# Performance work log

Hardware: AMD Instinct MI355X
Metric: run time of the kernel (lower is better)

## Reference

```python
import jax, jax.numpy as jnp
import numpy as np

T_STEPS = 500
NHEAD = 4
L_TRANS = 2

def _pe(L, D):
    pos = np.arange(L)[:, None].astype(np.float32)
    i = np.arange(D // 2)[None, :].astype(np.float32)
    ang = pos / np.power(10000.0, 2.0 * i / D)
    pe = np.zeros((L, D), np.float32)
    pe[:, 0::2] = np.sin(ang)
    pe[:, 1::2] = np.cos(ang)
    return jnp.asarray(pe)

def _ln(x, g, b):
    m = x.mean(-1, keepdims=True)
    v = ((x - m) ** 2).mean(-1, keepdims=True)
    return (x - m) / jnp.sqrt(v + 1e-5) * g + b

def _gcn(A, X, W1, b1, W2, b2, W3, b3):
    h = jax.nn.relu((A @ X) @ W1 + b1)
    h = jax.nn.relu((A @ h) @ W2 + b2)
    return (A @ h) @ W3 + b3

def _mha(h, Wq, bq, Wk, bk, Wv, bv, Wo, bo):
    B, L, D = h.shape
    dh = D // NHEAD
    q = (h @ Wq + bq).reshape(B, L, NHEAD, dh)
    k = (h @ Wk + bk).reshape(B, L, NHEAD, dh)
    v = (h @ Wv + bv).reshape(B, L, NHEAD, dh)
    s = jnp.einsum('blhd,bmhd->bhlm', q, k) / jnp.sqrt(jnp.float32(dh))
    a = jax.nn.softmax(s, axis=-1)
    o = jnp.einsum('bhlm,bmhd->blhd', a, v).reshape(B, L, D)
    return o @ Wo + bo


def setup_inputs() -> dict:
    key = jax.random.key(0)
    ks = jax.random.split(key, 24)
    N_FP, N_WORD, DIM, HID = 10000, 4096, 20, 512
    HD1, HD2, LOUT, TDIM, FF = 128, 64, 3, 20, 2048
    N_ATOMS, N_RES, N_EDGES = 256, 4096, 65536
    w = lambda k, shp, s=0.05: jax.random.normal(k, shp, jnp.float32) * s
    idx_aa = jax.random.randint(ks[0], (N_RES,), 0, 20)
    x = jax.nn.one_hot(idx_aa, 20, dtype=jnp.float32)  # node one-hots
    adj_s = (jax.random.uniform(ks[1], (N_ATOMS, N_ATOMS)) < 0.1).astype(jnp.float32)
    return dict(
        x=x,
        smileadjacency=adj_s,
        emb_fp=w(ks[2], (N_FP, DIM)),
        emb_word=w(ks[3], (N_WORD, HID), 0.02),
        gW1=w(ks[4], (DIM, HD1)), gb1=jnp.zeros((HD1,), jnp.float32),
        gW2=w(ks[5], (HD1, HD2)), gb2=jnp.zeros((HD2,), jnp.float32),
        gW3=w(ks[6], (HD2, DIM)), gb3=jnp.zeros((DIM,), jnp.float32),
        Wq=w(ks[7], (L_TRANS, HID, HID)), bq=jnp.zeros((L_TRANS, HID), jnp.float32),
        Wk=w(ks[8], (L_TRANS, HID, HID)), bk=jnp.zeros((L_TRANS, HID), jnp.float32),
        Wv=w(ks[9], (L_TRANS, HID, HID)), bv=jnp.zeros((L_TRANS, HID), jnp.float32),
        Wo=w(ks[10], (L_TRANS, HID, HID)), bo=jnp.zeros((L_TRANS, HID), jnp.float32),
        ln1g=jnp.ones((L_TRANS, HID), jnp.float32), ln1b=jnp.zeros((L_TRANS, HID), jnp.float32),
        Wff1=w(ks[11], (L_TRANS, HID, FF)), bff1=jnp.zeros((L_TRANS, FF), jnp.float32),
        Wff2=w(ks[12], (L_TRANS, FF, HID)), bff2=jnp.zeros((L_TRANS, HID), jnp.float32),
        ln2g=jnp.ones((L_TRANS, HID), jnp.float32), ln2b=jnp.zeros((L_TRANS, HID), jnp.float32),
        Wproj=w(ks[13], (HID, DIM)), bproj=jnp.zeros((DIM,), jnp.float32),
        Wout=w(ks[14], (LOUT, 4 * DIM, 4 * DIM)), bout=jnp.zeros((LOUT, 4 * DIM), jnp.float32),
        Wtime=w(ks[15], (1, TDIM)), btime=jnp.zeros((TDIM,), jnp.float32),
        fingerprints=jax.random.randint(ks[16], (N_ATOMS,), 0, N_FP),
        words=jax.random.randint(ks[17], (N_RES,), 0, N_WORD),
        batch=jnp.zeros((N_RES,), jnp.int32),
        edge_index=jax.random.randint(ks[18], (2, N_EDGES), 0, N_RES),
        t=250,
        layer_output=3,
        dropout=0,
    )


def reference(x, smileadjacency, emb_fp, emb_word, gW1, gb1, gW2, gb2, gW3, gb3,
              Wq, bq, Wk, bk, Wv, bv, Wo, bo, ln1g, ln1b, Wff1, bff1, Wff2, bff2,
              ln2g, ln2b, Wproj, bproj, Wout, bout, Wtime, btime,
              fingerprints, words, batch, edge_index, t, layer_output, dropout):
    # --- diffusion noise (cosine alpha_bar, blosum-style transition, uniform mixing) ---
    t_float = float(t) / T_STEPS
    s = 0.008
    ab = np.cos((t_float + s) / (1 + s) * np.pi / 2) ** 2 / (np.cos(s / (1 + s) * np.pi / 2) ** 2)
    ab = jnp.float32(ab)
    Qtb = ab * jnp.eye(20, dtype=jnp.float32) + (1.0 - ab) / 20.0  # [20,20]
    prob = jnp.einsum('nij,nj->ni', Qtb[None][batch], x[:, :20])    # [n,20]
    X_t = jax.random.categorical(jax.random.key(42), jnp.log(prob + 1e-9))
    X = jax.nn.one_hot(X_t, 20, dtype=jnp.float32)
    time_emb = jnp.array([[t_float]], jnp.float32) @ Wtime + btime  # [1,20]
    # --- substrate GCN ---
    fp_vec = emb_fp[fingerprints]                                   # [n_atoms, dim]
    sub = _gcn(smileadjacency, fp_vec, gW1, gb1, gW2, gb2, gW3, gb3).mean(0, keepdims=True)
    # --- sequence transformer ---
    h = emb_word[words][None] + _pe(words.shape[0], emb_word.shape[1])[None]  # [1,L,hid]
    for l in range(L_TRANS):
        a = _mha(h, Wq[l], bq[l], Wk[l], bk[l], Wv[l], bv[l], Wo[l], bo[l])
        h = _ln(h + a, ln1g[l], ln1b[l])
        ff = jax.nn.relu(h @ Wff1[l] + bff1[l]) @ Wff2[l] + bff2[l]
        h = _ln(h + ff, ln2g[l], ln2b[l])
    seq = (h[0] @ Wproj + bproj).mean(0, keepdims=True)             # [1,dim]
    # --- protein graph: vectorized adjacency scatter (replaces per-edge python loop) ---
    n = X.shape[0]
    adj = jnp.zeros((n, n), jnp.float32).at[edge_index[0], edge_index[1]].set(1.0)
    prot = _gcn(adj, X, gW1, gb1, gW2, gb2, gW3, gb3).mean(0, keepdims=True)
    # --- fusion head (dropout=0 / eval mode) ---
    cat = jnp.concatenate([sub, prot, seq, time_emb], axis=1)        # [1, 4*dim]
    for j in range(int(layer_output)):
        cat = jax.nn.relu(cat) @ Wout[j] + bout[j]
    cat = jax.nn.relu(cat)
    return (cat, seq)
```

## Files before the change

kernel.cpp:

```cpp
#include <hip/hip_runtime.h>
#include <math.h>

typedef unsigned short ushort_t;
typedef __attribute__((ext_vector_type(8))) short bf16x8;
typedef __attribute__((ext_vector_type(4))) float f32x4;

__device__ inline float bf2f(unsigned u) { return __uint_as_float((u & 0xffffu) << 16); }
__device__ inline ushort_t f2bf(float f) {
    unsigned u = __float_as_uint(f);
    return (ushort_t)((u + 0x7fffu + ((u >> 16) & 1u)) >> 16);
}
__device__ inline unsigned pack2(float a, float b) {
    return (unsigned)f2bf(a) | ((unsigned)f2bf(b) << 16);
}
__device__ inline void stv(float* p, float v) { *p = v; }
__device__ inline void stv(ushort_t* p, float v) { *p = f2bf(v); }
__device__ inline int guard_int(int raw, int lo, int hi) {
    if (raw >= lo && raw <= hi) return raw;
    float f = __int_as_float(raw);
    int v = (int)f;
    return (v >= lo && v <= hi) ? v : lo;
}

__device__ inline void tf2x32(unsigned k0, unsigned k1, unsigned x0, unsigned x1,
                              unsigned& o0, unsigned& o1) {
    unsigned ks2 = k0 ^ k1 ^ 0x1BD11BDAu;
    x0 += k0; x1 += k1;
#define TFR(r) { x0 += x1; x1 = (x1 << (r)) | (x1 >> (32 - (r))); x1 ^= x0; }
    TFR(13) TFR(15) TFR(26) TFR(6)  x0 += k1;  x1 += ks2 + 1u;
    TFR(17) TFR(29) TFR(16) TFR(24) x0 += ks2; x1 += k0 + 2u;
    TFR(13) TFR(15) TFR(26) TFR(6)  x0 += k0;  x1 += k1 + 3u;
    TFR(17) TFR(29) TFR(16) TFR(24) x0 += k1;  x1 += ks2 + 4u;
    TFR(13) TFR(15) TFR(26) TFR(6)  x0 += ks2; x1 += k0 + 5u;
#undef TFR
    o0 = x0; o1 = x1;
}

__global__ void k_sentinel(float* __restrict__ out, float val, int n) {
    int i = blockIdx.x * 128 + threadIdx.x;
    if (i < n) out[i] = val;
}

__global__ __launch_bounds__(256) void k_sample(const float* __restrict__ x,
                                                const int* __restrict__ t_ptr,
                                                float* __restrict__ X) {
    int i = blockIdx.x * 256 + threadIdx.x;
    if (i >= 4096) return;
    int tval = guard_int(t_ptr[0], 0, 500);
    double tf = (double)tval / 500.0;
    const double sc = 0.008;
    const double PI_HALF = 1.5707963267948966;
    double num = cos((tf + sc) / (1.0 + sc) * PI_HALF);
    double den = cos(sc / (1.0 + sc) * PI_HALF);
    float ab = (float)((num * num) / (den * den));
    float phi = (1.0f - ab) / 20.0f;
    float xv[20]; float sx = 0.f;
    for (int j = 0; j < 20; ++j) { xv[j] = x[i * 20 + j]; sx += xv[j]; }
    float best = -1e30f; int bj = 0;
    for (int j = 0; j < 20; ++j) {
        float prob = fmaxf(ab * xv[j] + phi * sx, 0.0f);
        float lp = logf(prob + 1e-9f);
        unsigned m = (unsigned)(i * 20 + j);
        unsigned o0, o1;
        tf2x32(0u, 42u, 0u, m, o0, o1);
        unsigned bits = o0 ^ o1;
        float u = __uint_as_float((bits >> 9) | 0x3f800000u) - 1.0f;
        if (u < 1.1754943508222875e-38f) u = 1.1754943508222875e-38f;
        float gmb = -logf(-logf(u));
        float z = lp + gmb;
        if (z > best) { best = z; bj = j; }
    }
    for (int j = 0; j < 20; ++j) X[i * 20 + j] = (j == bj) ? 1.0f : 0.0f;
}

__global__ __launch_bounds__(256) void k_gather_fp(const float* __restrict__ emb,
                                                   const int* __restrict__ idx,
                                                   float* __restrict__ out) {
    int i = blockIdx.x * 256 + threadIdx.x;
    if (i >= 256 * 20) return;
    int a = i / 20, d = i % 20;
    out[i] = emb[(size_t)idx[a] * 20 + d];
}

__global__ __launch_bounds__(256) void k_scatter_bits(const int* __restrict__ ei,
                                                      unsigned* __restrict__ bits) {
    int e = blockIdx.x * 256 + threadIdx.x;
    if (e >= 65536) return;
    int r = ei[e], c = ei[65536 + e];
    atomicOr(&bits[(size_t)r * 128 + (c >> 5)], 1u << (c & 31));
}

__global__ __launch_bounds__(256) void k_degree(const unsigned* __restrict__ BITS,
                                                float* __restrict__ deg) {
    int i = blockIdx.x * 256 + threadIdx.x;
    if (i >= 4096 * 128) return;
    unsigned bits = BITS[i];
    int base = (i & 127) * 32;
    while (bits) { int b = __ffs(bits) - 1; bits &= bits - 1; atomicAdd(&deg[base + b], 1.0f); }
}

__global__ __launch_bounds__(256) void k_embed(const float* __restrict__ embw,
                                               const int* __restrict__ words,
                                               float* __restrict__ H,
                                               ushort_t* __restrict__ Hb) {
    int idx = blockIdx.x * 256 + threadIdx.x;
    if (idx >= 4096 * 512) return;
    int pos = idx >> 9, d = idx & 511;
    float e = embw[(size_t)words[pos] * 512 + d];
    float expo = (float)(d >> 1) * (1.0f / 256.0f);
    float ang = (float)pos * exp2f(-expo * 13.287712379549449f);
    float pe = (d & 1) ? cosf(ang) : sinf(ang);
    float v = e + pe;
    H[idx] = v; Hb[idx] = f2bf(v);
}

__global__ __launch_bounds__(256) void k_colmean(const float* __restrict__ M, int R, int C,
                                                 float* __restrict__ out) {
    __shared__ float red[256];
    int c = blockIdx.x, t = threadIdx.x;
    float s = 0.f;
    for (int r = t; r < R; r += 256) s += M[(size_t)r * C + c];
    red[t] = s; __syncthreads();
    for (int o = 128; o; o >>= 1) { if (t < o) red[t] += red[t + o]; __syncthreads(); }
    if (t == 0) out[c] = red[0] / (float)R;
}

__global__ __launch_bounds__(256) void k_wcolsum(const float* __restrict__ M, int R, int C,
                                                 const float* __restrict__ w,
                                                 float* __restrict__ out) {
    __shared__ float red[256];
    int c = blockIdx.x, t = threadIdx.x;
    float s = 0.f;
    for (int r = t; r < R; r += 256) s += w[r] * M[(size_t)r * C + c];
    red[t] = s; __syncthreads();
    for (int o = 128; o; o >>= 1) { if (t < o) red[t] += red[t + o]; __syncthreads(); }
    if (t == 0) out[c] = red[0];
}

__global__ __launch_bounds__(256) void k_matvec20(int D, float scale,
                                                  const float* __restrict__ vec,
                                                  const float* __restrict__ W,
                                                  const float* __restrict__ bias,
                                                  float* __restrict__ out) {
    __shared__ float red[256];
    int c = blockIdx.x, t = threadIdx.x;
    float s = 0.f;
    for (int d = t; d < D; d += 256) s += vec[d] * W[(size_t)d * 20 + c];
    red[t] = s; __syncthreads();
    for (int o = 128; o; o >>= 1) { if (t < o) red[t] += red[t + o]; __syncthreads(); }
    if (t == 0) out[c] = red[0] * scale + bias[c];
}

__global__ void k_gather3(const float* __restrict__ a, const float* __restrict__ b,
                          const float* __restrict__ c, float* __restrict__ out) {
    int i = blockIdx.x * 256 + threadIdx.x;
    if (i >= 1536) return;
    out[i] = (i < 512) ? a[i] : (i < 1024) ? b[i - 512] : c[i - 1024];
}

__global__ __launch_bounds__(256) void k_castT(const float* __restrict__ in,
                                               ushort_t* __restrict__ out,
                                               int Kd, int Nd) {
    __shared__ float t[32][33];
    int bx = blockIdx.x * 32, by = blockIdx.y * 32;
    int tx = threadIdx.x & 31, ty = threadIdx.x >> 5;
#pragma unroll
    for (int i = 0; i < 4; ++i)
        t[ty + i * 8][tx] = in[(size_t)(by + ty + i * 8) * Nd + bx + tx];
    __syncthreads();
#pragma unroll
    for (int i = 0; i < 4; ++i)
        out[(size_t)(bx + ty + i * 8) * Kd + by + tx] = f2bf(t[tx][ty + i * 8]);
}

__global__ __launch_bounds__(256) void k_castT4(const float* __restrict__ in0,
                                                const float* __restrict__ in1,
                                                const float* __restrict__ in2,
                                                const float* __restrict__ in3,
                                                ushort_t* __restrict__ out) {
    __shared__ float t[32][33];
    int z = blockIdx.z;
    const float* in = (z == 0) ? in0 : (z == 1) ? in1 : (z == 2) ? in2 : in3;
    ushort_t* o = out + (size_t)z * 262144;
    int bx = blockIdx.x * 32, by = blockIdx.y * 32;
    int tx = threadIdx.x & 31, ty = threadIdx.x >> 5;
#pragma unroll
    for (int i = 0; i < 4; ++i)
        t[ty + i * 8][tx] = in[(size_t)(by + ty + i * 8) * 512 + bx + tx];
    __syncthreads();
#pragma unroll
    for (int i = 0; i < 4; ++i)
        o[(size_t)(bx + ty + i * 8) * 512 + by + tx] = f2bf(t[tx][ty + i * 8]);
}

template<int BN, bool RELU, bool VTR, typename TC>
__global__ __launch_bounds__(256) void k_gemm_mfma2(int M, int N, int K, int lda,
        const ushort_t* __restrict__ A,
        const ushort_t* __restrict__ Bt,
        TC* __restrict__ C, int ldc,
        const float* __restrict__ bias,
        ushort_t* __restrict__ VT) {
    constexpr int NJ = BN / 32;
    __shared__ ushort_t As[128][40];
    __shared__ ushort_t Bs[BN][40];
    int tid = threadIdx.x;
    int lane = tid & 63, wave = tid >> 6;
    int wr = wave >> 1, wc = wave & 1;
    int lrow = lane & 15, lq = lane >> 4;
    int br = blockIdx.y * 128, bc = blockIdx.x * BN;
    f32x4 acc[4][NJ];
#pragma unroll
    for (int i = 0; i < 4; ++i)
#pragma unroll
        for (int j = 0; j < NJ; ++j) { acc[i][j][0] = 0.f; acc[i][j][1] = 0.f; acc[i][j][2] = 0.f; acc[i][j][3] = 0.f; }
    int sr = tid >> 2, sseg = tid & 3;
    for (int k0 = 0; k0 < K; k0 += 32) {
#pragma unroll
        for (int it = 0; it < 2; ++it)
            *(uint4*)&As[sr + it * 64][sseg * 8] = *(const uint4*)&A[(size_t)(br + sr + it * 64) * lda + k0 + sseg * 8];
#pragma unroll
        for (int it = 0; it < BN / 64; ++it)
            *(uint4*)&Bs[sr + it * 64][sseg * 8] = *(const uint4*)&Bt[(size_t)(bc + sr + it * 64) * K + k0 + sseg * 8];
        __syncthreads();
        bf16x8 af[4], bfr[NJ];
#pragma unroll
        for (int i = 0; i < 4; ++i) af[i] = *(const bf16x8*)&As[wr * 64 + i * 16 + lrow][lq * 8];
#pragma unroll
        for (int j = 0; j < NJ; ++j) bfr[j] = *(const bf16x8*)&Bs[wc * (BN / 2) + j * 16 + lrow][lq * 8];
#pragma unroll
        for (int i = 0; i < 4; ++i)
#pragma unroll
            for (int j = 0; j < NJ; ++j)
                acc[i][j] = __builtin_amdgcn_mfma_f32_16x16x32_bf16(af[i], bfr[j], acc[i][j], 0, 0, 0);
        __syncthreads();
    }
#pragma unroll
    for (int i = 0; i < 4; ++i)
#pragma unroll
        for (int j = 0; j < NJ; ++j) {
            int col = bc + wc * (BN / 2) + j * 16 + lrow;
            float bv = bias ? bias[col] : 0.f;
            int row0 = br + wr * 64 + i * 16 + lq * 4;
            if (VTR && col >= 1024) {
                uint2 w;
                w.x = pack2(acc[i][j][0] + bv, acc[i][j][1] + bv);
                w.y = pack2(acc[i][j][2] + bv, acc[i][j][3] + bv);
                *(uint2*)&VT[(size_t)(col - 1024) * 4096 + row0] = w;
            } else {
#pragma unroll
                for (int r = 0; r < 4; ++r) {
                    float v = acc[i][j][r] + bv;
                    if (RELU) v = fmaxf(v, 0.f);
                    stv(&C[(size_t)(row0 + r) * ldc + col], v);
                }
            }
        }
}

template<bool RELU>
__global__ __launch_bounds__(256) void k_gemm_nn(int M, int N, int K,
        const float* __restrict__ A, int lda,
        const float* __restrict__ B, int ldb,
        float* __restrict__ C, int ldc,
        const float* __restrict__ bias) {
    __shared__ float As[16][65];
    __shared__ float Bs[16][65];
    int tid = threadIdx.x;
    int tx = tid & 15, ty = tid >> 4;
    int br = blockIdx.y * 64, bc = blockIdx.x * 64;
    float acc[4][4] = {};
    for (int k0 = 0; k0 < K; k0 += 16) {
#pragma unroll
        for (int c0 = 0; c0 < 4; ++c0) {
            int r = (tid >> 4) + c0 * 16, kk = tid & 15;
            int gr = br + r, gk = k0 + kk;
            As[kk][r] = (gr < M && gk < K) ? A[(size_t)gr * lda + gk] : 0.f;
        }
#pragma unroll
        for (int c0 = 0; c0 < 4; ++c0) {
            int col = tid & 63, kk = (tid >> 6) + c0 * 4;
            int gc = bc + col, gk = k0 + kk;
            Bs[kk][col] = (gc < N && gk < K) ? B[(size_t)gk * ldb + gc] : 0.f;
        }
        __syncthreads();
#pragma unroll
        for (int kk = 0; kk < 16; ++kk) {
            float av[4], bv[4];
#pragma unroll
            for (int i2 = 0; i2 < 4; ++i2) av[i2] = As[kk][ty + 16 * i2];
#pragma unroll
            for (int j2 = 0; j2 < 4; ++j2) bv[j2] = Bs[kk][tx + 16 * j2];
#pragma unroll
            for (int i2 = 0; i2 < 4; ++i2)
#pragma unroll
                for (int j2 = 0; j2 < 4; ++j2) acc[i2][j2] += av[i2] * bv[j2];
        }
        __syncthreads();
    }
#pragma unroll
    for (int i2 = 0; i2 < 4; ++i2)
#pragma unroll
        for (int j2 = 0; j2 < 4; ++j2) {
            int r = br + ty + 16 * i2, c = bc + tx + 16 * j2;
            if (r < M && c < N) {
                float v = acc[i2][j2];
                if (bias) v += bias[c];
                if (RELU) v = fmaxf(v, 0.f);
                C[(size_t)r * ldc + c] = v;
            }
        }
}

template<int NC, int CH>
__global__ __launch_bounds__(256) void k_spmm_wave(
        const unsigned* __restrict__ BITS,
        const float* __restrict__ B, int ldb,
        float* __restrict__ C, int ldc) {
    int gw = blockIdx.x * 4 + (threadIdx.x >> 6);
    int lane = threadIdx.x & 63;
    int row = gw / CH, cb = (gw % CH) * NC;
    if (row >= 4096) return;
    float acc[NC];
#pragma unroll
    for (int j = 0; j < NC; ++j) acc[j] = 0.f;
    const unsigned* bw = &BITS[(size_t)row * 128];
#pragma unroll
    for (int i = 0; i < 2; ++i) {
        int wd = lane * 2 + i;
        unsigned bits = bw[wd];
        int base = wd * 32;
        while (bits) {
            int b = __ffs(bits) - 1; bits &= bits - 1;
            const float* br = &B[(size_t)(base + b) * ldb + cb];
#pragma unroll
            for (int j = 0; j < NC; ++j) acc[j] += br[j];
        }
    }
#pragma unroll
    for (int j = 0; j < NC; ++j) {
#pragma unroll
        for (int off = 1; off < 64; off <<= 1) acc[j] += __shfl_xor(acc[j], off, 64);
    }
    if (lane == 0)
#pragma unroll
        for (int j = 0; j < NC; ++j) C[(size_t)row * ldc + cb + j] = acc[j];
}

__global__ __launch_bounds__(256) void k_flash(const ushort_t* __restrict__ Qg, int ldq,
                                               const ushort_t* __restrict__ Kg, int ldk,
                                               const ushort_t* __restrict__ VTg,
                                               ushort_t* __restrict__ OP0,
                                               ushort_t* __restrict__ OP12,
                                               float* __restrict__ Mp,
                                               float* __restrict__ Lp) {
    __shared__ ushort_t Ks[32][136];
    __shared__ ushort_t Vt[128][40];
    __shared__ ushort_t Ps[4][16][40];
    __shared__ float    as_[4][16];
    __shared__ float    ls_[4][16];
    const int tid = threadIdx.x;
    const int lane = tid & 63, wid = tid >> 6;
    const int lrow = lane & 15, lq = lane >> 4;
    const int qb = blockIdx.x * 64, hh = blockIdx.y, z = blockIdx.z;
    const int kt0 = z * 43, kt1 = (z == 2) ? 128 : kt0 + 43;
    const float scale = 0.08838834764831845f;
    bf16x8 qf[4];
    {
        const ushort_t* qrow = &Qg[(size_t)(qb + wid * 16 + lrow) * ldq + hh * 128 + lq * 8];
#pragma unroll
        for (int s = 0; s < 4; ++s) qf[s] = *(const bf16x8*)&qrow[s * 32];
    }
    f32x4 o[8];
#pragma unroll
    for (int ct = 0; ct < 8; ++ct) { o[ct][0] = 0.f; o[ct][1] = 0.f; o[ct][2] = 0.f; o[ct][3] = 0.f; }
    float m = -INFINITY, l = 0.f;
    for (int kt = kt0; kt < kt1; ++kt) {
#pragma unroll
        for (int i = 0; i < 2; ++i) {
            int sid = tid + i * 256;
            int r = sid >> 4, sg = sid & 15;
            *(uint4*)&Ks[r][sg * 8] = *(const uint4*)&Kg[(size_t)(kt * 32 + r) * ldk + hh * 128 + sg * 8];
            int d = sid >> 2, c8 = sid & 3;
            *(uint4*)&Vt[d][c8 * 8] = *(const uint4*)&VTg[(size_t)(hh * 128 + d) * 4096 + kt * 32 + c8 * 8];
        }
        __syncthreads();
        f32x4 sa[2];
#pragma unroll
        for (int c = 0; c < 2; ++c) { sa[c][0] = 0.f; sa[c][1] = 0.f; sa[c][2] = 0.f; sa[c][3] = 0.f; }
#pragma unroll
        for (int c = 0; c < 2; ++c)
#pragma unroll
            for (int st = 0; st < 4; ++st) {
                bf16x8 kf = *(const bf16x8*)&Ks[c * 16 + lrow][st * 32 + lq * 8];
                sa[c] = __builtin_amdgcn_mfma_f32_16x16x32_bf16(kf, qf[st], sa[c], 0, 0, 0);
            }
        float s[8];
        float tm = -INFINITY;
#pragma unroll
        for (int c = 0; c < 2; ++c)
#pragma unroll
            for (int r = 0; r < 4; ++r) { float v = sa[c][r] * scale; s[c * 4 + r] = v; tm = fmaxf(tm, v); }
        tm = fmaxf(tm, __shfl_xor(tm, 16));
        tm = fmaxf(tm, __shfl_xor(tm, 32));
        bool up = tm > m;
        float mn = up ? tm : m;
        float a = up ? __expf(m - mn) : 1.0f;
        float su = 0.f;
        float p[8];
#pragma unroll
        for (int i = 0; i < 8; ++i) { p[i] = __expf(s[i] - mn); su += p[i]; }
        su += __shfl_xor(su, 16);
        su += __shfl_xor(su, 32);
        m = mn; l = l * a + su;
#pragma unroll
        for (int c = 0; c < 2; ++c) {
            uint2 w;
            w.x = pack2(p[c * 4 + 0], p[c * 4 + 1]);
            w.y = pack2(p[c * 4 + 2], p[c * 4 + 3]);
            *(uint2*)&Ps[wid][lrow][c * 16 + lq * 4] = w;
        }
        if (__any(up)) {
            if (lq == 0) as_[wid][lrow] = a;
            __builtin_amdgcn_s_waitcnt(0);
            float av[4];
#pragma unroll
            for (int r = 0; r < 4; ++r) av[r] = as_[wid][lq * 4 + r];
#pragma unroll
            for (int ct = 0; ct < 8; ++ct)
#pragma unroll
                for (int r = 0; r < 4; ++r) o[ct][r] *= av[r];
        } else {
            __builtin_amdgcn_s_waitcnt(0);
        }
        bf16x8 pf = *(const bf16x8*)&Ps[wid][lrow][lq * 8];
#pragma unroll
        for (int ct = 0; ct < 8; ++ct) {
            bf16x8 vf = *(const bf16x8*)&Vt[ct * 16 + lrow][lq * 8];
            o[ct] = __builtin_amdgcn_mfma_f32_16x16x32_bf16(pf, vf, o[ct], 0, 0, 0);
        }
        __syncthreads();
    }
    if (lq == 0) {
        Mp[(size_t)(z * 4 + hh) * 4096 + qb + wid * 16 + lrow] = m;
        Lp[(size_t)(z * 4 + hh) * 4096 + qb + wid * 16 + lrow] = l;
    }
    ushort_t* ob = (z == 0) ? OP0 : OP12 + (size_t)(z - 1) * 2097152;
#pragma unroll
    for (int ct = 0; ct < 8; ++ct)
#pragma unroll
        for (int r = 0; r < 4; ++r)
            ob[(size_t)(qb + wid * 16 + lq * 4 + r) * 512 + hh * 128 + ct * 16 + lrow] = f2bf(o[ct][r]);
}

__global__ __launch_bounds__(256) void k_fcomb(ushort_t* __restrict__ OP0,
                                               const ushort_t* __restrict__ OP12,
                                               const float* __restrict__ Mp,
                                               const float* __restrict__ Lp) {
    int idx = blockIdx.x * 256 + threadIdx.x;
    if (idx >= 4096 * 512) return;
    int row = idx >> 9, col = idx & 511;
    int hh = col >> 7;
    float m0 = Mp[hh * 4096 + row], m1 = Mp[(4 + hh) * 4096 + row], m2 = Mp[(8 + hh) * 4096 + row];
    float l0 = Lp[hh * 4096 + row], l1 = Lp[(4 + hh) * 4096 + row], l2 = Lp[(8 + hh) * 4096 + row];
    float mm = fmaxf(m0, fmaxf(m1, m2));
    float w0 = __expf(m0 - mm), w1 = __expf(m1 - mm), w2 = __expf(m2 - mm);
    float denom = l0 * w0 + l1 * w1 + l2 * w2;
    float o0 = bf2f(OP0[idx]), o1 = bf2f(OP12[idx]), o2 = bf2f(OP12[2097152 + idx]);
    OP0[idx] = f2bf((o0 * w0 + o1 * w1 + o2 * w2) / denom);
}

__global__ __launch_bounds__(256) void k_add_ln(const float* __restrict__ A,
                                                const float* __restrict__ B,
                                                float* __restrict__ O,
                                                ushort_t* __restrict__ Ob,
                                                const float* __restrict__ g,
                                                const float* __restrict__ b) {
    __shared__ float xr[512];
    __shared__ float red[256];
    int row = blockIdx.x, t = threadIdx.x;
    const float* a = A + (size_t)row * 512;
    const float* bb = B + (size_t)row * 512;
    float ls = 0.f;
    for (int j = t; j < 512; j += 256) { float v = a[j] + bb[j]; xr[j] = v; ls += v; }
    red[t] = ls; __syncthreads();
    for (int o = 128; o; o >>= 1) { if (t < o) red[t] += red[t + o]; __syncthreads(); }
    float mean = red[0] / 512.0f; __syncthreads();
    float lv = 0.f;
    for (int j = t; j < 512; j += 256) { float d = xr[j] - mean; lv += d * d; }
    red[t] = lv; __syncthreads();
    for (int o = 128; o; o >>= 1) { if (t < o) red[t] += red[t + o]; __syncthreads(); }
    float inv = 1.0f / sqrtf(red[0] / 512.0f + 1e-5f);
    float* o_ = O + (size_t)row * 512;
    ushort_t* ob = Ob + (size_t)row * 512;
    for (int j = t; j < 512; j += 256) {
        float v = (xr[j] - mean) * inv * g[j] + b[j];
        o_[j] = v; ob[j] = f2bf(v);
    }
}

__global__ __launch_bounds__(128) void k_fusion(const float* __restrict__ subv,
                                                const float* __restrict__ protv,
                                                const float* __restrict__ seqv,
                                                const float* __restrict__ Wtime,
                                                const float* __restrict__ btime,
                                                const float* __restrict__ Wout,
                                                const float* __restrict__ bout,
                                                const int* __restrict__ t_ptr,
                                                const int* __restrict__ lo_ptr,
                                                float* __restrict__ out) {
    __shared__ float cat[80];
    int t = threadIdx.x;
    int tval = guard_int(t_ptr[0], 0, 500);
    int L    = guard_int(lo_ptr[0], 0, 3);
    float tf = (float)((double)tval / 500.0);
    if (t < 20) {
        cat[t] = subv[t];
        cat[20 + t] = protv[t];
        cat[40 + t] = seqv[t];
        cat[60 + t] = tf * Wtime[t] + btime[t];
    }
    __syncthreads();
    for (int j = 0; j < L; ++j) {
        float acc = 0.f;
        if (t < 80) {
            for (int i2 = 0; i2 < 80; ++i2)
                acc += fmaxf(cat[i2], 0.f) * Wout[(size_t)j * 6400 + i2 * 80 + t];
            acc += bout[j * 80 + t];
        }
        __syncthreads();
        if (t < 80) cat[t] = acc;
        __syncthreads();
    }
    if (t < 80) out[t] = fmaxf(cat[t], 0.f);
    if (t < 20) out[80 + t] = seqv[t];
}

extern "C" void kernel_launch(void* const* d_in, const int* in_sizes, int n_in,
                              void* d_out, int out_size, void* d_ws, size_t ws_size,
                              hipStream_t stream) {
    static const int EXP[39] = {
        81920, 65536, 200000, 2097152, 2560, 128, 8192, 64, 1280, 20,
        524288, 1024, 524288, 1024, 524288, 1024, 524288, 1024, 1024, 1024,
        2097152, 4096, 2097152, 1024, 1024, 1024, 10240, 20, 19200, 240,
        20, 20, 256, 4096, 4096, 131072, 1, 1, 1 };
    float code = 0.f;
    if (n_in != 39) code = 900.f;
    else {
        for (int i = 0; i < 39; ++i)
            if (in_sizes[i] != EXP[i]) { code = 500.f + 4.f * (float)i; break; }
    }
    const size_t REQ = (size_t)46 * 1024 * 1024;
    if (code == 0.f && ws_size < REQ) code = (float)(ws_size >> 20);
    float* out = (float*)d_out;
    if (code != 0.f) {
        k_sentinel<<<1, 128, 0, stream>>>(out, -code, out_size);
        return;
    }

    const float* x_in   = (const float*)d_in[0];
    const float* adjs_in= (const float*)d_in[1];
    const float* embfp  = (const float*)d_in[2];
    const float* embw   = (const float*)d_in[3];
    const float* gW1 = (const float*)d_in[4];  const float* gb1 = (const float*)d_in[5];
    const float* gW2 = (const float*)d_in[6];  const float* gb2 = (const float*)d_in[7];
    const float* gW3 = (const float*)d_in[8];  const float* gb3 = (const float*)d_in[9];
    const float* Wq  = (const float*)d_in[10]; const float* bq  = (const float*)d_in[11];
    const float* Wk  = (const float*)d_in[12]; const float* bk  = (const float*)d_in[13];
    const float* Wv  = (const float*)d_in[14]; const float* bv  = (const float*)d_in[15];
    const float* Wo  = (const float*)d_in[16]; const float* bo  = (const float*)d_in[17];
    const float* ln1g= (const float*)d_in[18]; const float* ln1b= (const float*)d_in[19];
    const float* Wff1= (const float*)d_in[20]; const float* bff1= (const float*)d_in[21];
    const float* Wff2= (const float*)d_in[22]; const float* bff2= (const float*)d_in[23];
    const float* ln2g= (const float*)d_in[24]; const float* ln2b= (const float*)d_in[25];
    const float* Wproj=(const float*)d_in[26]; const float* bproj=(const float*)d_in[27];
    const float* Woutw=(const float*)d_in[28]; const float* boutw=(const float*)d_in[29];
    const float* Wtime=(const float*)d_in[30]; const float* btime=(const float*)d_in[31];
    const int* fingerprints = (const int*)d_in[32];
    const int* words        = (const int*)d_in[33];
    const int* edge_index   = (const int*)d_in[35];
    const int* t_ptr        = (const int*)d_in[36];
    const int* lo_ptr       = (const int*)d_in[37];

    char* wsb = (char*)d_ws;
    float*    misc = (float*)wsb;
    float*    H    = (float*)(wsb + ((size_t)2  << 20));
    ushort_t* Hb   = (ushort_t*)(wsb + ((size_t)10 << 20));
    ushort_t* QKVb = (ushort_t*)(wsb + ((size_t)14 << 20));
    ushort_t* Ob   = (ushort_t*)(wsb + ((size_t)26 << 20));
    ushort_t* FFHb = (ushort_t*)(wsb + ((size_t)14 << 20));
    float*    T    = (float*)(wsb + ((size_t)30 << 20));
    ushort_t* OP12 = (ushort_t*)(wsb + ((size_t)30 << 20));
    ushort_t* Wscr = (ushort_t*)(wsb + ((size_t)38 << 20));
    ushort_t* VTg  = (ushort_t*)(wsb + ((size_t)42 << 20));
    unsigned* ADJB = (unsigned*)(wsb + ((size_t)26 << 20));
    float* pt0  = (float*)(wsb + ((size_t)14 << 20));
    float* ph1  = pt0 + 81920;
    float* pt1  = ph1 + 524288;
    float* ph2  = pt1 + 524288;
    float* Xoh  = misc;
    float* fpv  = misc + 81920;
    float* st0  = misc + 87040;
    float* sh1  = misc + 92160;
    float* st1  = misc + 124928;
    float* sh2  = misc + 157696;
    float* st2  = misc + 174080;
    float* sgo  = misc + 190464;
    float* subv = misc + 277504;
    float* protv= misc + 277536;
    float* seqv = misc + 277568;
    float* hmean= misc + 280000;
    float* wsum = misc + 281000;
    float* deg  = misc + 282000;
    float* bqkv = misc + 287000;
    float* Mp   = misc + 300000;
    float* Lp   = misc + 360000;

    auto g2 = [](int M, int N) { return dim3((unsigned)((N + 63) / 64), (unsigned)((M + 63) / 64), 1); };
    auto gm64  = [](int M, int N) { return dim3((unsigned)(N / 64), (unsigned)(M / 128), 1); };
    auto gm128 = [](int M, int N) { return dim3((unsigned)(N / 128), (unsigned)(M / 128), 1); };
    auto gt = [](int Kd, int Nd) { return dim3((unsigned)(Nd / 32), (unsigned)(Kd / 32), 1); };

    k_sample<<<16, 256, 0, stream>>>(x_in, t_ptr, Xoh);

    k_gather_fp<<<20, 256, 0, stream>>>(embfp, fingerprints, fpv);
    k_gemm_nn<false><<<g2(256, 20), 256, 0, stream>>>(256, 20, 256, adjs_in, 256, fpv, 20, st0, 20, nullptr);
    k_gemm_nn<true ><<<g2(256, 128), 256, 0, stream>>>(256, 128, 20, st0, 20, gW1, 128, sh1, 128, gb1);
    k_gemm_nn<false><<<g2(256, 128), 256, 0, stream>>>(256, 128, 256, adjs_in, 256, sh1, 128, st1, 128, nullptr);
    k_gemm_nn<true ><<<g2(256, 64), 256, 0, stream>>>(256, 64, 128, st1, 128, gW2, 64, sh2, 64, gb2);
    k_gemm_nn<false><<<g2(256, 64), 256, 0, stream>>>(256, 64, 256, adjs_in, 256, sh2, 64, st2, 64, nullptr);
    k_gemm_nn<false><<<g2(256, 20), 256, 0, stream>>>(256, 20, 64, st2, 64, gW3, 20, sgo, 20, gb3);
    k_colmean<<<20, 256, 0, stream>>>(sgo, 256, 20, subv);

    k_embed<<<8192, 256, 0, stream>>>(embw, words, H, Hb);
    for (int l = 0; l < 2; ++l) {
        k_castT4<<<dim3(16, 16, 4), 256, 0, stream>>>(Wq + (size_t)l * 262144, Wk + (size_t)l * 262144,
                                                      Wv + (size_t)l * 262144, Wo + (size_t)l * 262144, Wscr);
        k_gather3<<<6, 256, 0, stream>>>(bq + l * 512, bk + l * 512, bv + l * 512, bqkv);
        k_gemm_mfma2<64, false, true, ushort_t><<<gm64(4096, 1536), 256, 0, stream>>>(
            4096, 1536, 512, 512, Hb, Wscr, QKVb, 1536, bqkv, VTg);
        k_flash<<<dim3(64, 4, 3), 256, 0, stream>>>(QKVb, 1536, QKVb + 512, 1536, VTg, Ob, OP12, Mp, Lp);
        k_fcomb<<<8192, 256, 0, stream>>>(Ob, OP12, Mp, Lp);
        k_gemm_mfma2<64, false, false, float><<<gm64(4096, 512), 256, 0, stream>>>(
            4096, 512, 512, 512, Ob, Wscr + 786432, T, 512, bo + l * 512, nullptr);
        k_add_ln<<<4096, 256, 0, stream>>>(H, T, H, Hb, ln1g + l * 512, ln1b + l * 512);
        k_castT<<<gt(512, 2048), 256, 0, stream>>>(Wff1 + (size_t)l * 1048576, Wscr, 512, 2048);
        k_gemm_mfma2<128, true, false, ushort_t><<<gm128(4096, 2048), 256, 0, stream>>>(
            4096, 2048, 512, 512, Hb, Wscr, FFHb, 2048, bff1 + l * 2048, nullptr);
        k_castT<<<gt(2048, 512), 256, 0, stream>>>(Wff2 + (size_t)l * 1048576, Wscr, 2048, 512);
        k_gemm_mfma2<64, false, false, float><<<gm64(4096, 512), 256, 0, stream>>>(
            4096, 512, 2048, 2048, FFHb, Wscr, T, 512, bff2 + l * 512, nullptr);
        k_add_ln<<<4096, 256, 0, stream>>>(H, T, H, Hb, ln2g + l * 512, ln2b + l * 512);
    }

    k_colmean<<<512, 256, 0, stream>>>(H, 4096, 512, hmean);
    k_matvec20<<<20, 256, 0, stream>>>(512, 1.0f, hmean, Wproj, bproj, seqv);

    hipMemsetAsync(ADJB, 0, (size_t)4096 * 128 * 4, stream);
    hipMemsetAsync(deg, 0, 4096 * 4, stream);
    k_scatter_bits<<<256, 256, 0, stream>>>(edge_index, ADJB);
    k_spmm_wave<20, 1><<<1024, 256, 0, stream>>>(ADJB, Xoh, 20, pt0, 20);
    k_gemm_nn<true ><<<g2(4096, 128), 256, 0, stream>>>(4096, 128, 20, pt0, 20, gW1, 128, ph1, 128, gb1);
    k_spmm_wave<32, 4><<<4096, 256, 0, stream>>>(ADJB, ph1, 128, pt1, 128);
    k_gemm_nn<true ><<<g2(4096, 64), 256, 0, stream>>>(4096, 64, 128, pt1, 128, gW2, 64, ph2, 64, gb2);
    k_degree<<<2048, 256, 0, stream>>>(ADJB, deg);
    k_wcolsum<<<64, 256, 0, stream>>>(ph2, 4096, 64, deg, wsum);
    k_matvec20<<<20, 256, 0, stream>>>(64, 1.0f / 4096.0f, wsum, gW3, gb3, protv);

    k_fusion<<<1, 128, 0, stream>>>(subv, protv, seqv, Wtime, btime, Woutw, boutw, t_ptr, lo_ptr, out);
}
```

Measured before the change: 863.9 us.

## Double-buffer K/V tiles in flash attention and use 64x64 GEMM for N=512 projections

The flash-attention kernel now double-buffers its K and V shared-memory tiles. It prefetches the next tile into registers while computing the current one, then writes it to the other buffer before a single barrier, which removes one sync per iteration and hides global load latency. Separately, a new 64x64-tile MFMA GEMM replaces the 128x64 kernel for the output and FF2 projections (N=512), doubling the block count to improve CU occupancy. The costs are extra LDS and register pressure in flash, and less data reuse per block in the smaller GEMM tiles.

```diff
diff --git a/kernel.cpp b/kernel.cpp
--- a/kernel.cpp
+++ b/kernel.cpp
@@ -257,6 +257,58 @@
         }
 }
 
+template<bool RELU, typename TC>
+__global__ __launch_bounds__(256) void k_gemm_mfma64(int M, int N, int K, int lda,
+        const ushort_t* __restrict__ A,
+        const ushort_t* __restrict__ Bt,
+        TC* __restrict__ C, int ldc,
+        const float* __restrict__ bias) {
+    __shared__ ushort_t As[64][40];
+    __shared__ ushort_t Bs[64][40];
+    int tid = threadIdx.x;
+    int lane = tid & 63, wave = tid >> 6;
+    int wr = wave >> 1, wc = wave & 1;
+    int lrow = lane & 15, lq = lane >> 4;
+    int br = blockIdx.y * 64, bc = blockIdx.x * 64;
+    f32x4 acc[2][2];
+#pragma unroll
+    for (int i = 0; i < 2; ++i)
+#pragma unroll
+        for (int j = 0; j < 2; ++j) { acc[i][j][0] = 0.f; acc[i][j][1] = 0.f; acc[i][j][2] = 0.f; acc[i][j][3] = 0.f; }
+    int sr = tid >> 2, sseg = tid & 3;
+    for (int k0 = 0; k0 < K; k0 += 32) {
+        *(uint4*)&As[sr][sseg * 8] = *(const uint4*)&A[(size_t)(br + sr) * lda + k0 + sseg * 8];
+        *(uint4*)&Bs[sr][sseg * 8] = *(const uint4*)&Bt[(size_t)(bc + sr) * K + k0 + sseg * 8];
+        __syncthreads();
+        bf16x8 af[2], bfr[2];
+#pragma unroll
+        for (int i = 0; i < 2; ++i) {
+            af[i]  = *(const bf16x8*)&As[wr * 32 + i * 16 + lrow][lq * 8];
+            bfr[i] = *(const bf16x8*)&Bs[wc * 32 + i * 16 + lrow][lq * 8];
+        }
+#pragma unroll
+        for (int i = 0; i < 2; ++i)
+#pragma unroll
+            for (int j = 0; j < 2; ++j)
+                acc[i][j] = __builtin_amdgcn_mfma_f32_16x16x32_bf16(af[i], bfr[j], acc[i][j], 0, 0, 0);
+        __syncthreads();
+    }
+#pragma unroll
+    for (int i = 0; i < 2; ++i)
+#pragma unroll
+        for (int j = 0; j < 2; ++j) {
+            int col = bc + wc * 32 + j * 16 + lrow;
+            float bv = bias ? bias[col] : 0.f;
+#pragma unroll
+            for (int r = 0; r < 4; ++r) {
+                int row = br + wr * 32 + i * 16 + lq * 4 + r;
+                float v = acc[i][j][r] + bv;
+                if (RELU) v = fmaxf(v, 0.f);
+                stv(&C[(size_t)row * ldc + col], v);
+            }
+        }
+}
+
 template<bool RELU>
 __global__ __launch_bounds__(256) void k_gemm_nn(int M, int N, int K,
         const float* __restrict__ A, int lda,
@@ -353,8 +405,8 @@
                                                ushort_t* __restrict__ OP12,
                                                float* __restrict__ Mp,
                                                float* __restrict__ Lp) {
-    __shared__ ushort_t Ks[32][136];
-    __shared__ ushort_t Vt[128][40];
+    __shared__ ushort_t Ks[2][32][136];
+    __shared__ ushort_t Vt[2][128][40];
     __shared__ ushort_t Ps[4][16][40];
     __shared__ float    as_[4][16];
     __shared__ float    ls_[4][16];
@@ -364,6 +416,8 @@
     const int qb = blockIdx.x * 64, hh = blockIdx.y, z = blockIdx.z;
     const int kt0 = z * 43, kt1 = (z == 2) ? 128 : kt0 + 43;
     const float scale = 0.08838834764831845f;
+    const int s0r = tid >> 4, sg = tid & 15;
+    const int d0 = tid >> 2, c8 = tid & 3;
     bf16x8 qf[4];
     {
         const ushort_t* qrow = &Qg[(size_t)(qb + wid * 16 + lrow) * ldq + hh * 128 + lq * 8];
@@ -374,16 +428,24 @@
 #pragma unroll
     for (int ct = 0; ct < 8; ++ct) { o[ct][0] = 0.f; o[ct][1] = 0.f; o[ct][2] = 0.f; o[ct][3] = 0.f; }
     float m = -INFINITY, l = 0.f;
+    {
+        *(uint4*)&Ks[0][s0r][sg * 8]      = *(const uint4*)&Kg[(size_t)(kt0 * 32 + s0r) * ldk + hh * 128 + sg * 8];
+        *(uint4*)&Ks[0][s0r + 16][sg * 8] = *(const uint4*)&Kg[(size_t)(kt0 * 32 + s0r + 16) * ldk + hh * 128 + sg * 8];
+        *(uint4*)&Vt[0][d0][c8 * 8]       = *(const uint4*)&VTg[(size_t)(hh * 128 + d0) * 4096 + kt0 * 32 + c8 * 8];
+        *(uint4*)&Vt[0][d0 + 64][c8 * 8]  = *(const uint4*)&VTg[(size_t)(hh * 128 + d0 + 64) * 4096 + kt0 * 32 + c8 * 8];
+    }
+    __syncthreads();
+    int buf = 0;
     for (int kt = kt0; kt < kt1; ++kt) {
-#pragma unroll
-        for (int i = 0; i < 2; ++i) {
-            int sid = tid + i * 256;
-            int r = sid >> 4, sg = sid & 15;
-            *(uint4*)&Ks[r][sg * 8] = *(const uint4*)&Kg[(size_t)(kt * 32 + r) * ldk + hh * 128 + sg * 8];
-            int d = sid >> 2, c8 = sid & 3;
-            *(uint4*)&Vt[d][c8 * 8] = *(const uint4*)&VTg[(size_t)(hh * 128 + d) * 4096 + kt * 32 + c8 * 8];
-        }
-        __syncthreads();
+        uint4 kr0, kr1, vr0, vr1;
+        const bool pf = (kt + 1 < kt1);
+        if (pf) {
+            int kn = kt + 1;
+            kr0 = *(const uint4*)&Kg[(size_t)(kn * 32 + s0r) * ldk + hh * 128 + sg * 8];
+            kr1 = *(const uint4*)&Kg[(size_t)(kn * 32 + s0r + 16) * ldk + hh * 128 + sg * 8];
+            vr0 = *(const uint4*)&VTg[(size_t)(hh * 128 + d0) * 4096 + kn * 32 + c8 * 8];
+            vr1 = *(const uint4*)&VTg[(size_t)(hh * 128 + d0 + 64) * 4096 + kn * 32 + c8 * 8];
+        }
         f32x4 sa[2];
 #pragma unroll
         for (int c = 0; c < 2; ++c) { sa[c][0] = 0.f; sa[c][1] = 0.f; sa[c][2] = 0.f; sa[c][3] = 0.f; }
@@ -391,7 +453,7 @@
         for (int c = 0; c < 2; ++c)
 #pragma unroll
             for (int st = 0; st < 4; ++st) {
-                bf16x8 kf = *(const bf16x8*)&Ks[c * 16 + lrow][st * 32 + lq * 8];
+                bf16x8 kf = *(const bf16x8*)&Ks[buf][c * 16 + lrow][st * 32 + lq * 8];
                 sa[c] = __builtin_amdgcn_mfma_f32_16x16x32_bf16(kf, qf[st], sa[c], 0, 0, 0);
             }
         float s[8];
@@ -432,13 +494,20 @@
         } else {
             __builtin_amdgcn_s_waitcnt(0);
         }
-        bf16x8 pf = *(const bf16x8*)&Ps[wid][lrow][lq * 8];
+        bf16x8 pfv = *(const bf16x8*)&Ps[wid][lrow][lq * 8];
 #pragma unroll
         for (int ct = 0; ct < 8; ++ct) {
-            bf16x8 vf = *(const bf16x8*)&Vt[ct * 16 + lrow][lq * 8];
-            o[ct] = __builtin_amdgcn_mfma_f32_16x16x32_bf16(pf, vf, o[ct], 0, 0, 0);
-        }
-        __syncthreads();
+            bf16x8 vf = *(const bf16x8*)&Vt[buf][ct * 16 + lrow][lq * 8];
+            o[ct] = __builtin_amdgcn_mfma_f32_16x16x32_bf16(pfv, vf, o[ct], 0, 0, 0);
+        }
+        if (pf) {
+            *(uint4*)&Ks[buf ^ 1][s0r][sg * 8]      = kr0;
+            *(uint4*)&Ks[buf ^ 1][s0r + 16][sg * 8] = kr1;
+            *(uint4*)&Vt[buf ^ 1][d0][c8 * 8]       = vr0;
+            *(uint4*)&Vt[buf ^ 1][d0 + 64][c8 * 8]  = vr1;
+        }
+        __syncthreads();
+        buf ^= 1;
     }
     if (lq == 0) {
         Mp[(size_t)(z * 4 + hh) * 4096 + qb + wid * 16 + lrow] = m;
@@ -618,6 +687,7 @@
     auto g2 = [](int M, int N) { return dim3((unsigned)((N + 63) / 64), (unsigned)((M + 63) / 64), 1); };
     auto gm64  = [](int M, int N) { return dim3((unsigned)(N / 64), (unsigned)(M / 128), 1); };
     auto gm128 = [](int M, int N) { return dim3((unsigned)(N / 128), (unsigned)(M / 128), 1); };
+    auto gs64  = [](int M, int N) { return dim3((unsigned)(N / 64), (unsigned)(M / 64), 1); };
     auto gt = [](int Kd, int Nd) { return dim3((unsigned)(Nd / 32), (unsigned)(Kd / 32), 1); };
 
     k_sample<<<16, 256, 0, stream>>>(x_in, t_ptr, Xoh);
@@ -640,15 +710,15 @@
             4096, 1536, 512, 512, Hb, Wscr, QKVb, 1536, bqkv, VTg);
         k_flash<<<dim3(64, 4, 3), 256, 0, stream>>>(QKVb, 1536, QKVb + 512, 1536, VTg, Ob, OP12, Mp, Lp);
         k_fcomb<<<8192, 256, 0, stream>>>(Ob, OP12, Mp, Lp);
-        k_gemm_mfma2<64, false, false, float><<<gm64(4096, 512), 256, 0, stream>>>(
-            4096, 512, 512, 512, Ob, Wscr + 786432, T, 512, bo + l * 512, nullptr);
+        k_gemm_mfma64<false, float><<<gs64(4096, 512), 256, 0, stream>>>(
+            4096, 512, 512, 512, Ob, Wscr + 786432, T, 512, bo + l * 512);
         k_add_ln<<<4096, 256, 0, stream>>>(H, T, H, Hb, ln1g + l * 512, ln1b + l * 512);
         k_castT<<<gt(512, 2048), 256, 0, stream>>>(Wff1 + (size_t)l * 1048576, Wscr, 512, 2048);
         k_gemm_mfma2<128, true, false, ushort_t><<<gm128(4096, 2048), 256, 0, stream>>>(
             4096, 2048, 512, 512, Hb, Wscr, FFHb, 2048, bff1 + l * 2048, nullptr);
         k_castT<<<gt(2048, 512), 256, 0, stream>>>(Wff2 + (size_t)l * 1048576, Wscr, 2048, 512);
-        k_gemm_mfma2<64, false, false, float><<<gm64(4096, 512), 256, 0, stream>>>(
-            4096, 512, 2048, 2048, FFHb, Wscr, T, 512, bff2 + l * 512, nullptr);
+        k_gemm_mfma64<false, float><<<gs64(4096, 512), 256, 0, stream>>>(
+            4096, 512, 2048, 2048, FFHb, Wscr, T, 512, bff2 + l * 512);
         k_add_ln<<<4096, 256, 0, stream>>>(H, T, H, Hb, ln2g + l * 512, ln2b + l * 512);
     }
 
```

Result: no change. 855.8 us (-0.9%).
